# Kernel tuning notes

Hardware: AMD Instinct MI355X
Metric: run time of the kernel (lower is better)

The kernel has to match this reference:

```python
import jax, jax.numpy as jnp
import numpy as np

B, P, E, H, L = 16, 500, 128, 8, 3
N = P + 1
HD = E // H
LEAKY = 0.2
LN_EPS = 1e-5


def setup_inputs() -> dict:
    key = jax.random.key(0)
    ks = jax.random.split(key, 12)
    depot_xy = jax.random.uniform(ks[0], (B, 1, 2), dtype=jnp.float32)
    node_xy_demand_TW = jax.random.uniform(ks[1], (B, P, 5), dtype=jnp.float32)
    # random adjacency with guaranteed self-loops (avoids all -inf softmax rows)
    adj = jax.random.uniform(ks[2], (B, N, N)) > 0.5
    adj_mask = adj | jnp.eye(N, dtype=bool)[None]
    # embedding layers (nn.Linear: y = x @ W^T + b; we store W as (in, out))
    dep_W = jax.random.normal(ks[3], (2, E), dtype=jnp.float32) * 0.1
    dep_b = jnp.zeros((E,), dtype=jnp.float32)
    node_W = jax.random.normal(ks[4], (5, E), dtype=jnp.float32) * 0.1
    node_b = jnp.zeros((E,), dtype=jnp.float32)
    # per-layer GAT params, stacked over L
    W = jax.random.normal(ks[5], (L, E, E), dtype=jnp.float32) * (1.0 / np.sqrt(E))
    attn = jax.random.normal(ks[6], (L, H, 2 * HD), dtype=jnp.float32) * 0.1
    ln_g = jnp.ones((L, E), dtype=jnp.float32)
    ln_b = jnp.zeros((L, E), dtype=jnp.float32)
    return dict(depot_xy=depot_xy, node_xy_demand_TW=node_xy_demand_TW,
                adj_mask=adj_mask, dep_W=dep_W, dep_b=dep_b,
                node_W=node_W, node_b=node_b, W=W, attn=attn,
                ln_g=ln_g, ln_b=ln_b)


def _layernorm(x, g, b):
    mu = jnp.mean(x, axis=-1, keepdims=True)
    var = jnp.var(x, axis=-1, keepdims=True)
    return (x - mu) * jax.lax.rsqrt(var + LN_EPS) * g + b


def _gat_layer(x, adj_mask, Wl, attn_l, g, b):
    # x: (B,N,E)
    xW = x @ Wl                                   # (B,N,E)
    xWh = xW.reshape(B, N, H, HD)
    a1, a2 = attn_l[:, :HD], attn_l[:, HD:]       # (H,HD) each
    # concat-score factorization: e_ij = <a1, xW_i> + <a2, xW_j>
    ei = jnp.einsum('bnhd,hd->bnh', xWh, a1)      # (B,N,H)
    ej = jnp.einsum('bnhd,hd->bnh', xWh, a2)
    e = ei[:, :, None, :] + ej[:, None, :, :]     # (B,N,N,H)
    e = jnp.where(e >= 0, e, LEAKY * e)           # LeakyReLU
    e = jnp.where(adj_mask[..., None], e, -jnp.inf)
    alpha = jax.nn.softmax(e, axis=2)             # over source nodes j
    out = jnp.einsum('bijh,bjhd->bihd', alpha, xWh).reshape(B, N, E)
    out = _layernorm(out + xW, g, b)
    return jax.nn.elu(out)


def reference(depot_xy, node_xy_demand_TW, adj_mask, dep_W, dep_b,
              node_W, node_b, W, attn, ln_g, ln_b):
    depot_emb = depot_xy @ dep_W + dep_b          # (B,1,E)
    node_emb = node_xy_demand_TW @ node_W + node_b  # (B,P,E)
    x = jnp.concatenate([depot_emb, node_emb], axis=1)  # (B,N,E)
    for l in range(L):
        x = _gat_layer(x, adj_mask, W[l], attn[l], ln_g[l], ln_b[l])
    return x
```

## Files before the change

### kernel.cpp

```cpp
#include <hip/hip_runtime.h>
#include <hip/hip_cooperative_groups.h>
#include <hip/hip_bf16.h>
#include <math.h>

namespace cg = cooperative_groups;

#define Bn 16
#define Pn 500
#define Nn 501
#define En 128
#define Hn 8
#define Ln 3
#define ROWS (Bn*Nn)
#define LN_EPS 1e-5f

typedef __attribute__((ext_vector_type(8))) short bf16x8;
typedef __attribute__((ext_vector_type(4))) float f32x4;

__device__ inline float bfu2f(unsigned short u) {
  union { unsigned u32; float f; } c; c.u32 = ((unsigned)u) << 16; return c.f;
}
__device__ inline unsigned short f2bfu(float x) {
  __hip_bfloat16 h = __float2bfloat16(x);
  union { __hip_bfloat16 hh; unsigned short u; } c; c.hh = h; return c.u;
}

#define UNI_BYTES 141312
#define EJL_OFF   133120

__global__ __launch_bounds__(1024, 4) void mega_kernel(
    const float* __restrict__ depot, const float* __restrict__ node,
    const int* __restrict__ adj,
    const float* __restrict__ depW, const float* __restrict__ depB,
    const float* __restrict__ nodeW, const float* __restrict__ nodeB,
    const float* __restrict__ W, const float* __restrict__ attnw,
    const float* __restrict__ lng, const float* __restrict__ lnb,
    float* __restrict__ out,
    unsigned short* __restrict__ xwT0, unsigned short* __restrict__ ejT0,
    unsigned short* __restrict__ xwT1, unsigned short* __restrict__ ejT1) {
  cg::grid_group gg = cg::this_grid();

  __shared__ float xt[32][132];
  __shared__ float eit[32][8];
  __shared__ unsigned adjw[32][17];
  __shared__ __align__(16) char uni[UNI_BYTES];
  float* Bs = (float*)uni;
  unsigned short* VtT = (unsigned short*)uni;
  unsigned short* ejl = (unsigned short*)(uni + EJL_OFF);
  float* oout = (float*)uni;

  const int blk = blockIdx.x;
  const int t = threadIdx.x;
  const int b = blk >> 4;
  const int i0 = (blk & 15) << 5;
  const int rowb = b * Nn + i0;
  const int nval = (Nn - i0) < 32 ? (Nn - i0) : 32;
  const int wave = t >> 6, lane = t & 63;

#pragma unroll
  for (int r2 = 0; r2 < 2; ++r2) {
    int r = wave * 2 + r2;
    int grow = rowb + r; if (grow >= ROWS) grow = ROWS - 1;
    const int* ar = adj + (size_t)grow * Nn;
    int v[8];
#pragma unroll
    for (int s = 0; s < 8; ++s) {
      int col = s * 64 + lane;
      v[s] = (col < Nn) ? ar[col] : 0;
    }
#pragma unroll
    for (int s = 0; s < 8; ++s) {
      unsigned long long mk = __ballot(v[s] != 0);
      if (lane == 0) {
        adjw[r][2 * s]     = (unsigned)(mk & 0xffffffffull);
        adjw[r][2 * s + 1] = (unsigned)(mk >> 32);
      }
    }
  }
#pragma unroll
  for (int s = 0; s < 4; ++s) {
    int idx = t + s * 1024;
    int r = idx >> 7, e = idx & 127;
    int n = i0 + r;
    float v = 0.f;
    if (r < nval) {
      if (n == 0) {
        v = depB[e] + depot[b * 2 + 0] * depW[0 * En + e]
                    + depot[b * 2 + 1] * depW[1 * En + e];
      } else {
        const float* np_ = node + ((size_t)b * Pn + (n - 1)) * 5;
        v = nodeB[e];
#pragma unroll
        for (int k = 0; k < 5; k++) v += np_[k] * nodeW[k * En + e];
      }
    }
    xt[r][e] = v;
  }

  for (int l = 0; l < Ln; ++l) {
    const float* Wl = W + (size_t)l * En * En;
    const float* al = attnw + (size_t)l * Hn * 32;
    const float* g  = lng + (size_t)l * En;
    const float* bb = lnb + (size_t)l * En;
    unsigned short* xwT = (l & 1) ? xwT1 : xwT0;
    unsigned short* ejT = (l & 1) ? ejT1 : ejT0;

#pragma unroll
    for (int s = 0; s < 4; ++s) {
      int fidx = t + s * 1024;
      int r = fidx >> 5, c4 = (fidx & 31) << 2;
      *(f32x4*)&Bs[r * 132 + c4] = *(const f32x4*)&Wl[r * 128 + c4];
    }
    __syncthreads();

    {
      int tc = t & 31, tr = t >> 5;
      f32x4 a0 = {0.f, 0.f, 0.f, 0.f};
      for (int kk = 0; kk < 128; ++kk) {
        f32x4 bv = *(f32x4*)&Bs[kk * 132 + (tc << 2)];
        a0 += bv * xt[tr][kk];
      }
      __syncthreads();
      f32x4 z4 = {0.f, 0.f, 0.f, 0.f};
      *(f32x4*)&xt[tr][tc << 2] = (tr < nval) ? a0 : z4;
    }
    __syncthreads();

    if (t < 512) {
      int c = t >> 2, jg = t & 3;
      bf16x8 pk;
#pragma unroll
      for (int u = 0; u < 8; ++u) pk[u] = (short)f2bfu(xt[jg * 8 + u][c]);
      *(bf16x8*)&xwT[((size_t)(b * 128 + c)) * 512 + i0 + jg * 8] = pk;
    }
    if (t < 512) {
      int r = t >> 4, rest = t & 15, h = rest >> 1, sel = rest & 1;
      const float* av = al + h * 32 + sel * 16;
      float ss = 0.f;
#pragma unroll
      for (int d = 0; d < 16; ++d) ss += xt[r][h * 16 + d] * av[d];
      if (sel) ejT[((size_t)(b * 8 + h)) * 512 + i0 + r] = f2bfu(r < nval ? ss : 0.f);
      else     eit[r][h] = ss;
    }
    gg.sync();

#pragma unroll
    for (int s = 0; s < 8; ++s) {
      int idx = t + s * 1024;
      int c = idx >> 6, j8 = (idx & 63) << 3;
      *(bf16x8*)&VtT[c * 520 + j8] =
          *(const bf16x8*)&xwT[((size_t)(b * 128 + c)) * 512 + j8];
    }
    if (t < 512) {
      int hh = t >> 6, j8 = (t & 63) << 3;
      *(bf16x8*)&ejl[hh * 512 + j8] =
          *(const bf16x8*)&ejT[((size_t)(b * 8 + hh)) * 512 + j8];
    }
    __syncthreads();

    {
      const int h = wave >> 1;
      const int rg = wave & 1;
      const int li = lane & 15, lg = lane >> 4;
      const int r0 = rg << 4;
      float eiv0 = eit[r0 + li][h];
      f32x4 acc0 = {0.f, 0.f, 0.f, 0.f};
      float m0 = -1e30f, l0 = 0.f;

      for (int jt = 0; jt < 8; ++jt) {
        int j0 = jt << 6;
        float sc0[2][8];
#pragma unroll
        for (int kw = 0; kw < 2; ++kw) {
          int jb = j0 + (kw << 5) + (lg << 3);
          bf16x8 ev = *(bf16x8*)&ejl[h * 512 + jb];
          unsigned mb0 = (adjw[r0 + li][(jt << 1) + kw] >> (lg << 3)) & 0xffu;
#pragma unroll
          for (int e = 0; e < 8; ++e) {
            float ejv = bfu2f((unsigned short)ev[e]);
            float s0 = eiv0 + ejv; s0 = fmaxf(s0, 0.2f * s0);
            sc0[kw][e] = ((mb0 >> e) & 1u) ? s0 : -INFINITY;
          }
        }
        float tm0 = -INFINITY;
#pragma unroll
        for (int kw = 0; kw < 2; ++kw)
#pragma unroll
          for (int e = 0; e < 8; ++e) tm0 = fmaxf(tm0, sc0[kw][e]);
        tm0 = fmaxf(tm0, __shfl_xor(tm0, 16));
        tm0 = fmaxf(tm0, __shfl_xor(tm0, 32));
        float mn0 = fmaxf(m0, tm0);
        float fr0 = __expf(m0 - mn0);
        m0 = mn0;

        float ts0 = 0.f;
        bf16x8 pah0[2], pal0[2];
#pragma unroll
        for (int kw = 0; kw < 2; ++kw)
#pragma unroll
          for (int e = 0; e < 8; ++e) {
            float p0 = __expf(sc0[kw][e] - mn0);
            ts0 += p0;
            unsigned short h0 = f2bfu(p0);
            pah0[kw][e] = (short)h0;
            pal0[kw][e] = (short)f2bfu(p0 - bfu2f(h0));
          }
        ts0 += __shfl_xor(ts0, 16);
        ts0 += __shfl_xor(ts0, 32);
        l0 = l0 * fr0 + ts0;

        int base = lg << 2;
#pragma unroll
        for (int r = 0; r < 4; ++r) acc0[r] *= __shfl(fr0, base + r);

#pragma unroll
        for (int kw = 0; kw < 2; ++kw) {
          bf16x8 vb = *(bf16x8*)&VtT[(h * 16 + li) * 520 + j0 + (kw << 5) + (lg << 3)];
          acc0 = __builtin_amdgcn_mfma_f32_16x16x32_bf16(pah0[kw], vb, acc0, 0, 0, 0);
          acc0 = __builtin_amdgcn_mfma_f32_16x16x32_bf16(pal0[kw], vb, acc0, 0, 0, 0);
        }
      }
      __syncthreads();

      int base = lg << 2;
#pragma unroll
      for (int r = 0; r < 4; ++r) {
        float d0 = __shfl(l0, base + r);
        oout[(r0 + base + r) * 132 + h * 16 + li] = acc0[r] / d0;
      }
    }
    __syncthreads();

    {
      int row = t >> 5;
      int c0 = (t & 31) << 2;
      bool valid = row < nval;
      float4 o1 = *(float4*)&oout[row * 132 + c0];
      float4 x1 = *(float4*)&xt[row][c0];
      float y[4] = {o1.x + x1.x, o1.y + x1.y, o1.z + x1.z, o1.w + x1.w};
      float sum = 0.f, sq = 0.f;
#pragma unroll
      for (int u = 0; u < 4; ++u) { sum += y[u]; sq += y[u] * y[u]; }
#pragma unroll
      for (int mk = 1; mk <= 16; mk <<= 1) {
        sum += __shfl_xor(sum, mk);
        sq  += __shfl_xor(sq, mk);
      }
      float mu = sum * (1.f / 128.f);
      float var = sq * (1.f / 128.f) - mu * mu;
      float rs = rsqrtf(var + LN_EPS);
      const float4 g1 = *(const float4*)&g[c0];
      const float4 b1 = *(const float4*)&bb[c0];
      float gv[4] = {g1.x, g1.y, g1.z, g1.w};
      float bv[4] = {b1.x, b1.y, b1.z, b1.w};
      float zo[4];
#pragma unroll
      for (int u = 0; u < 4; ++u) {
        float z = (y[u] - mu) * rs * gv[u] + bv[u];
        zo[u] = (z > 0.f) ? z : expm1f(z);
      }
      if (l == Ln - 1) {
        if (valid) {
          float* op = &out[((size_t)(rowb + row)) * En + c0];
          *(float4*)op = make_float4(zo[0], zo[1], zo[2], zo[3]);
        }
      } else {
#pragma unroll
        for (int u = 0; u < 4; ++u) xt[row][c0 + u] = valid ? zo[u] : 0.f;
      }
    }
    __syncthreads();
  }
}

extern "C" void kernel_launch(void* const* d_in, const int* in_sizes, int n_in,
                              void* d_out, int out_size, void* d_ws, size_t ws_size,
                              hipStream_t stream) {
  const float* depot = (const float*)d_in[0];
  const float* node  = (const float*)d_in[1];
  const int*   adj   = (const int*)d_in[2];
  const float* depW  = (const float*)d_in[3];
  const float* depB  = (const float*)d_in[4];
  const float* nodeW = (const float*)d_in[5];
  const float* nodeB = (const float*)d_in[6];
  const float* W     = (const float*)d_in[7];
  const float* attnw = (const float*)d_in[8];
  const float* lng   = (const float*)d_in[9];
  const float* lnb   = (const float*)d_in[10];
  float* out = (float*)d_out;

  const size_t XW_ELEMS = (size_t)16 * 128 * 512;
  const size_t EJ_ELEMS = (size_t)16 * 8 * 512;
  unsigned short* xwT0 = (unsigned short*)d_ws;
  unsigned short* ejT0 = xwT0 + XW_ELEMS;
  unsigned short* xwT1 = ejT0 + EJ_ELEMS;
  unsigned short* ejT1 = xwT1 + XW_ELEMS;

  void* args[] = {
    (void*)&depot, (void*)&node, (void*)&adj,
    (void*)&depW, (void*)&depB, (void*)&nodeW, (void*)&nodeB,
    (void*)&W, (void*)&attnw, (void*)&lng, (void*)&lnb,
    (void*)&out, (void*)&xwT0, (void*)&ejT0, (void*)&xwT1, (void*)&ejT1
  };
  hipLaunchCooperativeKernel((const void*)mega_kernel, dim3(256), dim3(1024),
                             args, 0, stream);
}
```

Measured before the change: 281.5 us.

## Use split-bf16 MFMA for projection and stream V from global with prefetch

Replaces the scalar FP32 LDS-staged projection GEMM with bf16 MFMA, splitting values into hi/lo parts (three products) to keep near-FP32 accuracy, and reads W directly from global memory. It drops the large LDS staging of the transposed V matrix; each wave now loads its V fragments from global memory with a one-tile register prefetch inside the attention loop. LDS use shrinks a lot and one trailing block barrier is removed. The cost is extra conversion work and a dependence on L2/global latency for V instead of LDS.

```diff
diff --git a/kernel.cpp b/kernel.cpp
--- a/kernel.cpp
+++ b/kernel.cpp
@@ -15,6 +15,7 @@
 #define LN_EPS 1e-5f
 
 typedef __attribute__((ext_vector_type(8))) short bf16x8;
+typedef __attribute__((ext_vector_type(4))) short s16x4;
 typedef __attribute__((ext_vector_type(4))) float f32x4;
 
 __device__ inline float bfu2f(unsigned short u) {
@@ -24,9 +25,6 @@
   __hip_bfloat16 h = __float2bfloat16(x);
   union { __hip_bfloat16 hh; unsigned short u; } c; c.hh = h; return c.u;
 }
-
-#define UNI_BYTES 141312
-#define EJL_OFF   133120
 
 __global__ __launch_bounds__(1024, 4) void mega_kernel(
     const float* __restrict__ depot, const float* __restrict__ node,
@@ -43,11 +41,8 @@
   __shared__ float xt[32][132];
   __shared__ float eit[32][8];
   __shared__ unsigned adjw[32][17];
-  __shared__ __align__(16) char uni[UNI_BYTES];
-  float* Bs = (float*)uni;
-  unsigned short* VtT = (unsigned short*)uni;
-  unsigned short* ejl = (unsigned short*)(uni + EJL_OFF);
-  float* oout = (float*)uni;
+  __shared__ unsigned short ejl[8][512];
+  __shared__ float oout[32][132];
 
   const int blk = blockIdx.x;
   const int t = threadIdx.x;
@@ -56,6 +51,10 @@
   const int rowb = b * Nn + i0;
   const int nval = (Nn - i0) < 32 ? (Nn - i0) : 32;
   const int wave = t >> 6, lane = t & 63;
+  const int li = lane & 15, lg = lane >> 4;
+  const int h = wave >> 1;
+  const int rg = wave & 1;
+  const int r0 = rg << 4;
 
 #pragma unroll
   for (int r2 = 0; r2 < 2; ++r2) {
@@ -105,75 +104,86 @@
     unsigned short* xwT = (l & 1) ? xwT1 : xwT0;
     unsigned short* ejT = (l & 1) ? ejT1 : ejT0;
 
+    __syncthreads();
+
+    {
+      f32x4 acc = {0.f, 0.f, 0.f, 0.f};
+#pragma unroll
+      for (int ks = 0; ks < 4; ++ks) {
+        int kb = ks * 32 + lg * 8;
+        f32x4 x0 = *(f32x4*)&xt[r0 + li][kb];
+        f32x4 x1 = *(f32x4*)&xt[r0 + li][kb + 4];
+        bf16x8 a_hi, a_lo, b_hi, b_lo;
+#pragma unroll
+        for (int e = 0; e < 8; ++e) {
+          float v = (e < 4) ? x0[e] : x1[e - 4];
+          unsigned short hu = f2bfu(v);
+          a_hi[e] = (short)hu;
+          a_lo[e] = (short)f2bfu(v - bfu2f(hu));
+        }
+#pragma unroll
+        for (int e = 0; e < 8; ++e) {
+          float wv = Wl[(size_t)(kb + e) * 128 + h * 16 + li];
+          unsigned short hu = f2bfu(wv);
+          b_hi[e] = (short)hu;
+          b_lo[e] = (short)f2bfu(wv - bfu2f(hu));
+        }
+        acc = __builtin_amdgcn_mfma_f32_16x16x32_bf16(a_hi, b_hi, acc, 0, 0, 0);
+        acc = __builtin_amdgcn_mfma_f32_16x16x32_bf16(a_hi, b_lo, acc, 0, 0, 0);
+        acc = __builtin_amdgcn_mfma_f32_16x16x32_bf16(a_lo, b_hi, acc, 0, 0, 0);
+      }
+      __syncthreads();
+#pragma unroll
+      for (int r = 0; r < 4; ++r) oout[r0 + lg * 4 + r][h * 16 + li] = acc[r];
+      s16x4 pk;
+#pragma unroll
+      for (int r = 0; r < 4; ++r) pk[r] = (short)f2bfu(acc[r]);
+      *(s16x4*)&xwT[((size_t)(b * 128 + h * 16 + li)) * 512 + i0 + r0 + lg * 4] = pk;
+    }
+    __syncthreads();
 #pragma unroll
     for (int s = 0; s < 4; ++s) {
-      int fidx = t + s * 1024;
-      int r = fidx >> 5, c4 = (fidx & 31) << 2;
-      *(f32x4*)&Bs[r * 132 + c4] = *(const f32x4*)&Wl[r * 128 + c4];
-    }
-    __syncthreads();
-
-    {
-      int tc = t & 31, tr = t >> 5;
-      f32x4 a0 = {0.f, 0.f, 0.f, 0.f};
-      for (int kk = 0; kk < 128; ++kk) {
-        f32x4 bv = *(f32x4*)&Bs[kk * 132 + (tc << 2)];
-        a0 += bv * xt[tr][kk];
-      }
-      __syncthreads();
-      f32x4 z4 = {0.f, 0.f, 0.f, 0.f};
-      *(f32x4*)&xt[tr][tc << 2] = (tr < nval) ? a0 : z4;
-    }
-    __syncthreads();
-
+      int idx = t + s * 1024;
+      int r = idx >> 7, e = idx & 127;
+      xt[r][e] = oout[r][e];
+    }
+    __syncthreads();
     if (t < 512) {
-      int c = t >> 2, jg = t & 3;
-      bf16x8 pk;
-#pragma unroll
-      for (int u = 0; u < 8; ++u) pk[u] = (short)f2bfu(xt[jg * 8 + u][c]);
-      *(bf16x8*)&xwT[((size_t)(b * 128 + c)) * 512 + i0 + jg * 8] = pk;
-    }
-    if (t < 512) {
-      int r = t >> 4, rest = t & 15, h = rest >> 1, sel = rest & 1;
-      const float* av = al + h * 32 + sel * 16;
+      int r = t >> 4, rest = t & 15, hh = rest >> 1, sel = rest & 1;
+      const float* av = al + hh * 32 + sel * 16;
       float ss = 0.f;
 #pragma unroll
-      for (int d = 0; d < 16; ++d) ss += xt[r][h * 16 + d] * av[d];
-      if (sel) ejT[((size_t)(b * 8 + h)) * 512 + i0 + r] = f2bfu(r < nval ? ss : 0.f);
-      else     eit[r][h] = ss;
+      for (int d = 0; d < 16; ++d) ss += xt[r][hh * 16 + d] * av[d];
+      if (sel) ejT[((size_t)(b * 8 + hh)) * 512 + i0 + r] = f2bfu(r < nval ? ss : 0.f);
+      else     eit[r][hh] = ss;
     }
     gg.sync();
 
-#pragma unroll
-    for (int s = 0; s < 8; ++s) {
-      int idx = t + s * 1024;
-      int c = idx >> 6, j8 = (idx & 63) << 3;
-      *(bf16x8*)&VtT[c * 520 + j8] =
-          *(const bf16x8*)&xwT[((size_t)(b * 128 + c)) * 512 + j8];
-    }
+    const unsigned short* vbase = &xwT[((size_t)(b * 128 + h * 16 + li)) * 512];
+    bf16x8 vA0 = *(const bf16x8*)&vbase[lg * 8];
+    bf16x8 vA1 = *(const bf16x8*)&vbase[32 + lg * 8];
     if (t < 512) {
       int hh = t >> 6, j8 = (t & 63) << 3;
-      *(bf16x8*)&ejl[hh * 512 + j8] =
+      *(bf16x8*)&ejl[hh][j8] =
           *(const bf16x8*)&ejT[((size_t)(b * 8 + hh)) * 512 + j8];
     }
     __syncthreads();
 
     {
-      const int h = wave >> 1;
-      const int rg = wave & 1;
-      const int li = lane & 15, lg = lane >> 4;
-      const int r0 = rg << 4;
       float eiv0 = eit[r0 + li][h];
       f32x4 acc0 = {0.f, 0.f, 0.f, 0.f};
       float m0 = -1e30f, l0 = 0.f;
 
       for (int jt = 0; jt < 8; ++jt) {
-        int j0 = jt << 6;
+        bf16x8 vB0 = {}, vB1 = {};
+        if (jt < 7) {
+          vB0 = *(const bf16x8*)&vbase[(jt + 1) * 64 + lg * 8];
+          vB1 = *(const bf16x8*)&vbase[(jt + 1) * 64 + 32 + lg * 8];
+        }
         float sc0[2][8];
 #pragma unroll
         for (int kw = 0; kw < 2; ++kw) {
-          int jb = j0 + (kw << 5) + (lg << 3);
-          bf16x8 ev = *(bf16x8*)&ejl[h * 512 + jb];
+          bf16x8 ev = *(bf16x8*)&ejl[h][jt * 64 + kw * 32 + lg * 8];
           unsigned mb0 = (adjw[r0 + li][(jt << 1) + kw] >> (lg << 3)) & 0xffu;
 #pragma unroll
           for (int e = 0; e < 8; ++e) {
@@ -213,12 +223,11 @@
 #pragma unroll
         for (int r = 0; r < 4; ++r) acc0[r] *= __shfl(fr0, base + r);
 
-#pragma unroll
-        for (int kw = 0; kw < 2; ++kw) {
-          bf16x8 vb = *(bf16x8*)&VtT[(h * 16 + li) * 520 + j0 + (kw << 5) + (lg << 3)];
-          acc0 = __builtin_amdgcn_mfma_f32_16x16x32_bf16(pah0[kw], vb, acc0, 0, 0, 0);
-          acc0 = __builtin_amdgcn_mfma_f32_16x16x32_bf16(pal0[kw], vb, acc0, 0, 0, 0);
-        }
+        acc0 = __builtin_amdgcn_mfma_f32_16x16x32_bf16(pah0[0], vA0, acc0, 0, 0, 0);
+        acc0 = __builtin_amdgcn_mfma_f32_16x16x32_bf16(pal0[0], vA0, acc0, 0, 0, 0);
+        acc0 = __builtin_amdgcn_mfma_f32_16x16x32_bf16(pah0[1], vA1, acc0, 0, 0, 0);
+        acc0 = __builtin_amdgcn_mfma_f32_16x16x32_bf16(pal0[1], vA1, acc0, 0, 0, 0);
+        vA0 = vB0; vA1 = vB1;
       }
       __syncthreads();
 
@@ -226,7 +235,7 @@
 #pragma unroll
       for (int r = 0; r < 4; ++r) {
         float d0 = __shfl(l0, base + r);
-        oout[(r0 + base + r) * 132 + h * 16 + li] = acc0[r] / d0;
+        oout[r0 + base + r][h * 16 + li] = acc0[r] / d0;
       }
     }
     __syncthreads();
@@ -235,7 +244,7 @@
       int row = t >> 5;
       int c0 = (t & 31) << 2;
       bool valid = row < nval;
-      float4 o1 = *(float4*)&oout[row * 132 + c0];
+      float4 o1 = *(float4*)&oout[row][c0];
       float4 x1 = *(float4*)&xt[row][c0];
       float y[4] = {o1.x + x1.x, o1.y + x1.y, o1.z + x1.z, o1.w + x1.w};
       float sum = 0.f, sq = 0.f;
@@ -269,7 +278,6 @@
         for (int u = 0; u < 4; ++u) xt[row][c0 + u] = valid ? zo[u] : 0.f;
       }
     }
-    __syncthreads();
   }
 }
 
```

Result: faster. 266.6 us (-5.3%).
